# Kernel tuning notes

Hardware: AMD Instinct MI355X
Metric: run time of the kernel (lower is better)

## Reference

```python
import jax, jax.numpy as jnp
import numpy as np

D_MODEL = 1024
HEAD = 16
HEAD_DIM = D_MODEL // HEAD
BATCH = 2
SEQ = 2048


def setup_inputs() -> dict:
    key = jax.random.key(0)
    ks = jax.random.split(key, 11)
    s = 0.02
    return {
        "q": jax.random.normal(ks[0], (BATCH, SEQ, D_MODEL), dtype=jnp.float32),
        "k": jax.random.normal(ks[1], (BATCH, SEQ, D_MODEL), dtype=jnp.float32),
        "v": jax.random.normal(ks[2], (BATCH, SEQ, D_MODEL), dtype=jnp.float32),
        "w_q": jax.random.normal(ks[3], (D_MODEL, D_MODEL), dtype=jnp.float32) * s,
        "b_q": jnp.zeros((D_MODEL,), dtype=jnp.float32),
        "w_k": jax.random.normal(ks[4], (D_MODEL, D_MODEL), dtype=jnp.float32) * s,
        "b_k": jnp.zeros((D_MODEL,), dtype=jnp.float32),
        "w_v": jax.random.normal(ks[5], (D_MODEL, D_MODEL), dtype=jnp.float32) * s,
        "b_v": jnp.zeros((D_MODEL,), dtype=jnp.float32),
        "w_o": jax.random.normal(ks[6], (D_MODEL, D_MODEL), dtype=jnp.float32) * s,
        "b_o": jnp.zeros((D_MODEL,), dtype=jnp.float32),
    }


def reference(q, k, v, w_q, b_q, w_k, b_k, w_v, b_v, w_o, b_o):
    B, S, _ = q.shape
    # linear projections (torch Linear: x @ W^T + b)
    qp = q @ w_q.T + b_q
    kp = k @ w_k.T + b_k
    vp = v @ w_v.T + b_v
    # [B, S, H, Dh] -> [B, H, S, Dh]
    qh = qp.reshape(B, S, HEAD, HEAD_DIM).transpose(0, 2, 1, 3)
    kh = kp.reshape(B, S, HEAD, HEAD_DIM).transpose(0, 2, 1, 3)
    vh = vp.reshape(B, S, HEAD, HEAD_DIM).transpose(0, 2, 1, 3)
    # scaled dot-product attention with explicit score matrix
    scale = 1.0 / jnp.sqrt(jnp.float32(HEAD_DIM))
    scores = jnp.einsum("bhqd,bhkd->bhqk", qh, kh) * scale  # [B,H,S,S]
    attn = jax.nn.softmax(scores, axis=-1)
    z = jnp.einsum("bhqk,bhkd->bhqd", attn, vh)
    z = z.transpose(0, 2, 1, 3).reshape(B, S, D_MODEL)
    z = z @ w_o.T + b_o
    return (z, attn)
```

## Files before the change

kernel.cpp:

```cpp
#include <hip/hip_runtime.h>
#include <hip/hip_bf16.h>
#include <stdint.h>

#define D_MODEL 1024
#define NHEAD   16
#define HDIM    64
#define BATCH   2
#define SEQ     2048
#define BS_TOK  (BATCH*SEQ)

using bf16 = __hip_bfloat16;
typedef __attribute__((ext_vector_type(8))) short frag8;
typedef __attribute__((ext_vector_type(4))) float facc4;
typedef __attribute__((ext_vector_type(4))) float fvec4;

__device__ __forceinline__ void gld_lds16(const void* g, void* l) {
    __builtin_amdgcn_global_load_lds(
        reinterpret_cast<const __attribute__((address_space(1))) uint32_t*>(
            reinterpret_cast<uintptr_t>(g)),
        reinterpret_cast<__attribute__((address_space(3))) uint32_t*>(
            reinterpret_cast<uintptr_t>(l)),
        16, 0, 0);
}

__global__ __launch_bounds__(256) void cvt_multi(const float4* __restrict__ s0, const float4* __restrict__ s1,
                                                 const float4* __restrict__ s2, const float4* __restrict__ s3,
                                                 ushort4* __restrict__ d0, ushort4* __restrict__ d1,
                                                 ushort4* __restrict__ d2, ushort4* __restrict__ d3,
                                                 int n4, int nblk) {
    int t = blockIdx.x / nblk;
    int i = (blockIdx.x - t * nblk) * 256 + threadIdx.x;
    if (i >= n4) return;
    const float4* s = (t == 0) ? s0 : (t == 1) ? s1 : (t == 2) ? s2 : s3;
    ushort4*       d = (t == 0) ? d0 : (t == 1) ? d1 : (t == 2) ? d2 : d3;
    float4 v = s[i];
    bf16 a = __float2bfloat16(v.x), b = __float2bfloat16(v.y),
         c = __float2bfloat16(v.z), e = __float2bfloat16(v.w);
    ushort4 u;
    __builtin_memcpy(&u.x, &a, 2);
    __builtin_memcpy(&u.y, &b, 2);
    __builtin_memcpy(&u.z, &c, 2);
    __builtin_memcpy(&u.w, &e, 2);
    d[i] = u;
}

template<bool OUT_BF16, bool ROW_BIAS>
__device__ __forceinline__ void gemm_core(bf16* AsBuf, bf16* BsBuf,
                                          const bf16* __restrict__ A,
                                          const bf16* __restrict__ Bt,
                                          const float* __restrict__ bias,
                                          void* __restrict__ Cout,
                                          int M, int N, int K, int bx, int by) {
    const int tid  = threadIdx.x;
    const int lane = tid & 63, wave = tid >> 6;
    const int wm = wave >> 1, wn = wave & 1;
    const int L15 = lane & 15, quad = lane >> 4;
    const int m0 = by * 128, n0 = bx * 64;
    const int ar  = tid >> 3;
    const int acS = ((tid & 7) ^ (ar & 7)) * 8;

    const bf16* Agl[4];
    const bf16* Bgl[2];
#pragma unroll
    for (int q = 0; q < 4; q++) Agl[q] = A + (size_t)(m0 + q * 32 + ar) * K + acS;
#pragma unroll
    for (int q = 0; q < 2; q++) Bgl[q] = Bt + (size_t)(n0 + q * 32 + ar) * K + acS;

    const facc4 zero4 = {0.f, 0.f, 0.f, 0.f};
    facc4 acc[4][2];
#pragma unroll
    for (int mt = 0; mt < 4; mt++) { acc[mt][0] = zero4; acc[mt][1] = zero4; }

#define G_STAGE(BUF, KO) do {                                                   \
        _Pragma("unroll")                                                       \
        for (int q = 0; q < 4; q++)                                             \
            gld_lds16(Agl[q] + (KO), AsBuf + (BUF) * 8192 + q * 2048 + wave * 512); \
        _Pragma("unroll")                                                       \
        for (int q = 0; q < 2; q++)                                             \
            gld_lds16(Bgl[q] + (KO), BsBuf + (BUF) * 4096 + q * 2048 + wave * 512); \
    } while (0)

#define G_COMPUTE(BUF) do {                                                     \
        const bf16* Ab = AsBuf + (BUF) * 8192;                                  \
        const bf16* Bb = BsBuf + (BUF) * 4096;                                  \
        _Pragma("unroll")                                                       \
        for (int h = 0; h < 2; h++) {                                           \
            frag8 af[4], bfr[2];                                                \
            _Pragma("unroll")                                                   \
            for (int mt = 0; mt < 4; mt++) {                                    \
                int row = wm * 64 + mt * 16 + L15;                              \
                int c8 = (h * 4 + quad) ^ (row & 7);                            \
                af[mt] = *(const frag8*)(Ab + row * 64 + c8 * 8);               \
            }                                                                   \
            _Pragma("unroll")                                                   \
            for (int nt = 0; nt < 2; nt++) {                                    \
                int row = wn * 32 + nt * 16 + L15;                              \
                int c8 = (h * 4 + quad) ^ (row & 7);                            \
                bfr[nt] = *(const frag8*)(Bb + row * 64 + c8 * 8);              \
            }                                                                   \
            _Pragma("unroll")                                                   \
            for (int mt = 0; mt < 4; mt++)                                      \
                _Pragma("unroll")                                               \
                for (int nt = 0; nt < 2; nt++)                                  \
                    acc[mt][nt] = __builtin_amdgcn_mfma_f32_16x16x32_bf16(af[mt], bfr[nt], acc[mt][nt], 0, 0, 0); \
        }                                                                       \
    } while (0)

    G_STAGE(0, 0);
    __syncthreads();
    int cur = 0;
    for (int k0 = 64; k0 < K; k0 += 64) {
        G_STAGE(cur ^ 1, k0);
        G_COMPUTE(cur);
        __syncthreads();
        cur ^= 1;
    }
    G_COMPUTE(cur);

#pragma unroll
    for (int mt = 0; mt < 4; mt++)
#pragma unroll
        for (int nt = 0; nt < 2; nt++)
#pragma unroll
            for (int r = 0; r < 4; r++) {
                int row = m0 + wm * 64 + mt * 16 + quad * 4 + r;
                int col = n0 + wn * 32 + nt * 16 + L15;
                float v = acc[mt][nt][r] + (ROW_BIAS ? bias[row] : bias[col]);
                if (OUT_BF16) ((bf16*)Cout)[(size_t)row * N + col] = __float2bfloat16(v);
                else          ((float*)Cout)[(size_t)row * N + col] = v;
            }
#undef G_STAGE
#undef G_COMPUTE
}

template<bool OUT_BF16, bool ROW_BIAS>
__global__ __launch_bounds__(256) void gemm_bt(const bf16* __restrict__ A,
                                               const bf16* __restrict__ Bt,
                                               const float* __restrict__ bias,
                                               void* __restrict__ Cout,
                                               int M, int N, int K) {
    __shared__ bf16 As[2 * 8192];
    __shared__ bf16 Bs[2 * 4096];
    gemm_core<OUT_BF16, ROW_BIAS>(As, Bs, A, Bt, bias, Cout, M, N, K, blockIdx.x, blockIdx.y);
}

__global__ __launch_bounds__(256) void gemm_qk(const bf16* __restrict__ qA, const bf16* __restrict__ qW,
                                               const float* __restrict__ qb, bf16* __restrict__ qO,
                                               const bf16* __restrict__ kA, const bf16* __restrict__ kW,
                                               const float* __restrict__ kb, bf16* __restrict__ kO) {
    __shared__ bf16 As[2 * 8192];
    __shared__ bf16 Bs[2 * 4096];
    if (blockIdx.z == 0)
        gemm_core<true, false>(As, Bs, qA, qW, qb, qO, BS_TOK, D_MODEL, D_MODEL, blockIdx.x, blockIdx.y);
    else
        gemm_core<true, false>(As, Bs, kA, kW, kb, kO, BS_TOK, D_MODEL, D_MODEL, blockIdx.x, blockIdx.y);
}

__device__ __forceinline__ int pidx2(int row, int col) {
    int chunk = col >> 3;
    return row * 512 + (((chunk ^ (row & 7)) << 3) | (col & 7));
}

__global__ __launch_bounds__(256) void attn_kernel(const bf16* __restrict__ qp,
                                                   const bf16* __restrict__ kp,
                                                   const bf16* __restrict__ vT,
                                                   bf16* __restrict__ zbuf,
                                                   float* __restrict__ attn_out) {
    __shared__ bf16 ptile[16 * 512];
    __shared__ float sred[4][16];
    __shared__ float sinv[16];
    const int bid0 = blockIdx.x;
    const int bid = (bid0 & 7) * 512 + (bid0 >> 3);
    const int strip = bid & 127, bh = bid >> 7;
    const int b = bh >> 4, h = bh & 15;
    const int i0 = strip * 16;
    const int tid = threadIdx.x, lane = tid & 63, wave = tid >> 6;
    const int L15 = lane & 15, quad = lane >> 4;
    const float scale = 0.125f;

    frag8 aq0, aq1;
    {
        size_t base = (size_t)(b * SEQ + i0 + L15) * D_MODEL + h * HDIM + quad * 8;
        aq0 = *(const frag8*)(qp + base);
        aq1 = *(const frag8*)(qp + base + 32);
    }
    const facc4 zero4 = {0.f, 0.f, 0.f, 0.f};

    float sums[4] = {0.f, 0.f, 0.f, 0.f};
    for (int tt = 0; tt < 32; tt += 2) {
        int j0a = wave * 512 + tt * 16;
        size_t kba = (size_t)(b * SEQ + j0a + L15) * D_MODEL + h * HDIM + quad * 8;
        frag8 a0 = *(const frag8*)(kp + kba);
        frag8 a1 = *(const frag8*)(kp + kba + 32);
        frag8 c0 = *(const frag8*)(kp + kba + (size_t)16 * D_MODEL);
        frag8 c1 = *(const frag8*)(kp + kba + (size_t)16 * D_MODEL + 32);
        facc4 acca = zero4, accb = zero4;
        acca = __builtin_amdgcn_mfma_f32_16x16x32_bf16(aq0, a0, acca, 0, 0, 0);
        accb = __builtin_amdgcn_mfma_f32_16x16x32_bf16(aq0, c0, accb, 0, 0, 0);
        acca = __builtin_amdgcn_mfma_f32_16x16x32_bf16(aq1, a1, acca, 0, 0, 0);
        accb = __builtin_amdgcn_mfma_f32_16x16x32_bf16(aq1, c1, accb, 0, 0, 0);
#pragma unroll
        for (int r = 0; r < 4; r++)
            sums[r] += __expf(acca[r] * scale) + __expf(accb[r] * scale);
    }
#pragma unroll
    for (int m = 1; m <= 8; m <<= 1)
#pragma unroll
        for (int r = 0; r < 4; r++) sums[r] += __shfl_xor(sums[r], m, 64);
    if (L15 == 0) {
#pragma unroll
        for (int r = 0; r < 4; r++) sred[wave][quad * 4 + r] = sums[r];
    }
    __syncthreads();
    if (tid < 16) sinv[tid] = 1.0f / (sred[0][tid] + sred[1][tid] + sred[2][tid] + sred[3][tid]);
    __syncthreads();

    float invr[4];
#pragma unroll
    for (int r = 0; r < 4; r++) invr[r] = sinv[quad * 4 + r];

    facc4 zacc = zero4;
    const bf16* vrow = vT + (size_t)(h * HDIM + wave * 16 + L15) * BS_TOK + b * SEQ;
    const size_t obase = ((size_t)bh * SEQ + i0) * SEQ;

    for (int c = 0; c < 4; c++) {
#pragma unroll 2
        for (int tt = 0; tt < 8; tt++) {
            int jrel = wave * 128 + tt * 16;
            int j0 = c * 512 + jrel;
            size_t kb = (size_t)(b * SEQ + j0 + L15) * D_MODEL + h * HDIM + quad * 8;
            frag8 kf0 = *(const frag8*)(kp + kb);
            frag8 kf1 = *(const frag8*)(kp + kb + 32);
            facc4 acc = zero4;
            acc = __builtin_amdgcn_mfma_f32_16x16x32_bf16(aq0, kf0, acc, 0, 0, 0);
            acc = __builtin_amdgcn_mfma_f32_16x16x32_bf16(aq1, kf1, acc, 0, 0, 0);
            int colw = jrel + L15;
#pragma unroll
            for (int r = 0; r < 4; r++) {
                int row = quad * 4 + r;
                float a = __expf(acc[r] * scale) * invr[r];
                ptile[pidx2(row, colw)] = __float2bfloat16(a);
            }
        }
        __syncthreads();
#pragma unroll
        for (int it = 0; it < 4; it++) {
            int row = it * 4 + wave;
#pragma unroll
            for (int seg = 0; seg < 2; seg++) {
                int colb = seg * 256 + lane * 4;
                int chunk = colb >> 3, sub = colb & 7;
                const bf16* src = &ptile[row * 512 + (((chunk ^ (row & 7)) << 3) | sub)];
                fvec4 o = {__bfloat162float(src[0]), __bfloat162float(src[1]),
                           __bfloat162float(src[2]), __bfloat162float(src[3])};
                __builtin_nontemporal_store(o,
                    (fvec4*)(attn_out + obase + (size_t)row * SEQ + c * 512 + colb));
            }
        }
#pragma unroll 4
        for (int k0 = 0; k0 < 512; k0 += 32) {
            frag8 pa = *(const frag8*)&ptile[L15 * 512 + ((((k0 >> 3) + quad) ^ (L15 & 7)) << 3)];
            frag8 vb = *(const frag8*)(vrow + c * 512 + k0 + quad * 8);
            zacc = __builtin_amdgcn_mfma_f32_16x16x32_bf16(pa, vb, zacc, 0, 0, 0);
        }
        __syncthreads();
    }
#pragma unroll
    for (int r = 0; r < 4; r++) {
        size_t row = (size_t)(b * SEQ + i0 + quad * 4 + r);
        zbuf[row * D_MODEL + h * HDIM + wave * 16 + L15] = __float2bfloat16(zacc[r]);
    }
}

extern "C" void kernel_launch(void* const* d_in, const int* in_sizes, int n_in,
                              void* d_out, int out_size, void* d_ws, size_t ws_size,
                              hipStream_t stream) {
    const float* q   = (const float*)d_in[0];
    const float* k   = (const float*)d_in[1];
    const float* v   = (const float*)d_in[2];
    const float* w_q = (const float*)d_in[3];
    const float* b_q = (const float*)d_in[4];
    const float* w_k = (const float*)d_in[5];
    const float* b_k = (const float*)d_in[6];
    const float* w_v = (const float*)d_in[7];
    const float* b_v = (const float*)d_in[8];
    const float* w_o = (const float*)d_in[9];
    const float* b_o = (const float*)d_in[10];

    char* ws = (char*)d_ws;
    const size_t TOK = (size_t)BS_TOK * D_MODEL;
    const size_t WM  = (size_t)D_MODEL * D_MODEL;
    bf16* qbf  = (bf16*)(ws);
    bf16* kbf  = (bf16*)(ws + 8388608);
    bf16* vbf  = (bf16*)(ws + 16777216);
    bf16* wqb  = (bf16*)(ws + 25165824);
    bf16* wkb  = (bf16*)(ws + 27262976);
    bf16* wvb  = (bf16*)(ws + 29360128);
    bf16* wob  = (bf16*)(ws + 31457280);
    bf16* qp   = (bf16*)(ws + 33554432);
    bf16* kp   = (bf16*)(ws + 41943040);
    bf16* vT   = (bf16*)(ws + 50331648);
    bf16* zbf  = (bf16*)(ws + 58720256);

    float* z_out    = (float*)d_out;
    float* attn_out = (float*)d_out + (size_t)BATCH * SEQ * D_MODEL;

    int n4t = (int)(TOK / 4), n4w = (int)(WM / 4);
    int nbt = (n4t + 255) / 256, nbw = (n4w + 255) / 256;
    cvt_multi<<<3 * nbt, 256, 0, stream>>>((const float4*)q, (const float4*)k, (const float4*)v,
                                           (const float4*)v,
                                           (ushort4*)qbf, (ushort4*)kbf, (ushort4*)vbf,
                                           (ushort4*)vbf, n4t, nbt);
    cvt_multi<<<4 * nbw, 256, 0, stream>>>((const float4*)w_q, (const float4*)w_k,
                                           (const float4*)w_v, (const float4*)w_o,
                                           (ushort4*)wqb, (ushort4*)wkb, (ushort4*)wvb,
                                           (ushort4*)wob, n4w, nbw);

    dim3 gqk(D_MODEL / 64, BS_TOK / 128, 2);
    gemm_qk<<<gqk, 256, 0, stream>>>(qbf, wqb, b_q, qp, kbf, wkb, b_k, kp);
    dim3 g2(BS_TOK / 64, D_MODEL / 128);
    gemm_bt<true, true><<<g2, 256, 0, stream>>>(wvb, vbf, b_v, vT, D_MODEL, BS_TOK, D_MODEL);

    attn_kernel<<<BATCH * NHEAD * (SEQ / 16), 256, 0, stream>>>(qp, kp, vT, zbf, attn_out);

    dim3 g1(D_MODEL / 64, BS_TOK / 128);
    gemm_bt<false, false><<<g1, 256, 0, stream>>>(zbf, wob, b_o, z_out, BS_TOK, D_MODEL, D_MODEL);
}
```

Measured before the change: 913.0 us.

## Merge conversion and projection launches, double-buffer attention P tile

```diff
diff --git a/kernel.cpp b/kernel.cpp
--- a/kernel.cpp
+++ b/kernel.cpp
@@ -12,7 +12,6 @@
 using bf16 = __hip_bfloat16;
 typedef __attribute__((ext_vector_type(8))) short frag8;
 typedef __attribute__((ext_vector_type(4))) float facc4;
-typedef __attribute__((ext_vector_type(4))) float fvec4;
 
 __device__ __forceinline__ void gld_lds16(const void* g, void* l) {
     __builtin_amdgcn_global_load_lds(
@@ -23,19 +22,39 @@
         16, 0, 0);
 }
 
-__global__ __launch_bounds__(256) void cvt_multi(const float4* __restrict__ s0, const float4* __restrict__ s1,
-                                                 const float4* __restrict__ s2, const float4* __restrict__ s3,
-                                                 ushort4* __restrict__ d0, ushort4* __restrict__ d1,
-                                                 ushort4* __restrict__ d2, ushort4* __restrict__ d3,
-                                                 int n4, int nblk) {
-    int t = blockIdx.x / nblk;
-    int i = (blockIdx.x - t * nblk) * 256 + threadIdx.x;
+__device__ __forceinline__ void ldsbar() {
+    asm volatile("s_waitcnt lgkmcnt(0)" ::: "memory");
+    __builtin_amdgcn_sched_barrier(0);
+    __builtin_amdgcn_s_barrier();
+}
+
+__global__ __launch_bounds__(256) void cvt_all(const float* __restrict__ q, const float* __restrict__ k,
+                                               const float* __restrict__ v, const float* __restrict__ wq,
+                                               const float* __restrict__ wk, const float* __restrict__ wv,
+                                               const float* __restrict__ wo,
+                                               ushort* __restrict__ dq, ushort* __restrict__ dk,
+                                               ushort* __restrict__ dv, ushort* __restrict__ dwq,
+                                               ushort* __restrict__ dwk, ushort* __restrict__ dwv,
+                                               ushort* __restrict__ dwo,
+                                               int nbt, int n4t, int nbw, int n4w) {
+    int blk = blockIdx.x;
+    const float4* s; ushort4* d; int i, n4;
+    if (blk < 3 * nbt) {
+        int t = blk / nbt;
+        i = (blk - t * nbt) * 256 + threadIdx.x; n4 = n4t;
+        s = (const float4*)(t == 0 ? q : t == 1 ? k : v);
+        d = (ushort4*)(t == 0 ? dq : t == 1 ? dk : dv);
+    } else {
+        blk -= 3 * nbt;
+        int t = blk / nbw;
+        i = (blk - t * nbw) * 256 + threadIdx.x; n4 = n4w;
+        s = (const float4*)(t == 0 ? wq : t == 1 ? wk : t == 2 ? wv : wo);
+        d = (ushort4*)(t == 0 ? dwq : t == 1 ? dwk : t == 2 ? dwv : dwo);
+    }
     if (i >= n4) return;
-    const float4* s = (t == 0) ? s0 : (t == 1) ? s1 : (t == 2) ? s2 : s3;
-    ushort4*       d = (t == 0) ? d0 : (t == 1) ? d1 : (t == 2) ? d2 : d3;
-    float4 v = s[i];
-    bf16 a = __float2bfloat16(v.x), b = __float2bfloat16(v.y),
-         c = __float2bfloat16(v.z), e = __float2bfloat16(v.w);
+    float4 vv = s[i];
+    bf16 a = __float2bfloat16(vv.x), b = __float2bfloat16(vv.y),
+         c = __float2bfloat16(vv.z), e = __float2bfloat16(vv.w);
     ushort4 u;
     __builtin_memcpy(&u.x, &a, 2);
     __builtin_memcpy(&u.y, &b, 2);
@@ -133,6 +152,26 @@
 #undef G_COMPUTE
 }
 
+__global__ __launch_bounds__(256) void proj_all(const bf16* __restrict__ qA, const bf16* __restrict__ Wq,
+                                                const float* __restrict__ bq, bf16* __restrict__ qO,
+                                                const bf16* __restrict__ kA, const bf16* __restrict__ Wk,
+                                                const float* __restrict__ bk, bf16* __restrict__ kO,
+                                                const bf16* __restrict__ Wv, const bf16* __restrict__ vA,
+                                                const float* __restrict__ bv, bf16* __restrict__ vO) {
+    __shared__ bf16 As[2 * 8192];
+    __shared__ bf16 Bs[2 * 4096];
+    int id = blockIdx.x;
+    if (id < 512) {
+        gemm_core<true, false>(As, Bs, qA, Wq, bq, qO, BS_TOK, D_MODEL, D_MODEL, id & 15, id >> 4);
+    } else if (id < 1024) {
+        id -= 512;
+        gemm_core<true, false>(As, Bs, kA, Wk, bk, kO, BS_TOK, D_MODEL, D_MODEL, id & 15, id >> 4);
+    } else {
+        id -= 1024;
+        gemm_core<true, true>(As, Bs, Wv, vA, bv, vO, D_MODEL, BS_TOK, D_MODEL, id & 63, id >> 6);
+    }
+}
+
 template<bool OUT_BF16, bool ROW_BIAS>
 __global__ __launch_bounds__(256) void gemm_bt(const bf16* __restrict__ A,
                                                const bf16* __restrict__ Bt,
@@ -144,18 +183,6 @@
     gemm_core<OUT_BF16, ROW_BIAS>(As, Bs, A, Bt, bias, Cout, M, N, K, blockIdx.x, blockIdx.y);
 }
 
-__global__ __launch_bounds__(256) void gemm_qk(const bf16* __restrict__ qA, const bf16* __restrict__ qW,
-                                               const float* __restrict__ qb, bf16* __restrict__ qO,
-                                               const bf16* __restrict__ kA, const bf16* __restrict__ kW,
-                                               const float* __restrict__ kb, bf16* __restrict__ kO) {
-    __shared__ bf16 As[2 * 8192];
-    __shared__ bf16 Bs[2 * 4096];
-    if (blockIdx.z == 0)
-        gemm_core<true, false>(As, Bs, qA, qW, qb, qO, BS_TOK, D_MODEL, D_MODEL, blockIdx.x, blockIdx.y);
-    else
-        gemm_core<true, false>(As, Bs, kA, kW, kb, kO, BS_TOK, D_MODEL, D_MODEL, blockIdx.x, blockIdx.y);
-}
-
 __device__ __forceinline__ int pidx2(int row, int col) {
     int chunk = col >> 3;
     return row * 512 + (((chunk ^ (row & 7)) << 3) | (col & 7));
@@ -166,7 +193,7 @@
                                                    const bf16* __restrict__ vT,
                                                    bf16* __restrict__ zbuf,
                                                    float* __restrict__ attn_out) {
-    __shared__ bf16 ptile[16 * 512];
+    __shared__ bf16 ptile[2][16 * 512];
     __shared__ float sred[4][16];
     __shared__ float sinv[16];
     const int bid0 = blockIdx.x;
@@ -223,48 +250,50 @@
     const bf16* vrow = vT + (size_t)(h * HDIM + wave * 16 + L15) * BS_TOK + b * SEQ;
     const size_t obase = ((size_t)bh * SEQ + i0) * SEQ;
 
-    for (int c = 0; c < 4; c++) {
-#pragma unroll 2
-        for (int tt = 0; tt < 8; tt++) {
-            int jrel = wave * 128 + tt * 16;
-            int j0 = c * 512 + jrel;
-            size_t kb = (size_t)(b * SEQ + j0 + L15) * D_MODEL + h * HDIM + quad * 8;
-            frag8 kf0 = *(const frag8*)(kp + kb);
-            frag8 kf1 = *(const frag8*)(kp + kb + 32);
-            facc4 acc = zero4;
-            acc = __builtin_amdgcn_mfma_f32_16x16x32_bf16(aq0, kf0, acc, 0, 0, 0);
-            acc = __builtin_amdgcn_mfma_f32_16x16x32_bf16(aq1, kf1, acc, 0, 0, 0);
-            int colw = jrel + L15;
-#pragma unroll
-            for (int r = 0; r < 4; r++) {
-                int row = quad * 4 + r;
-                float a = __expf(acc[r] * scale) * invr[r];
-                ptile[pidx2(row, colw)] = __float2bfloat16(a);
-            }
-        }
-        __syncthreads();
-#pragma unroll
-        for (int it = 0; it < 4; it++) {
-            int row = it * 4 + wave;
-#pragma unroll
-            for (int seg = 0; seg < 2; seg++) {
-                int colb = seg * 256 + lane * 4;
-                int chunk = colb >> 3, sub = colb & 7;
-                const bf16* src = &ptile[row * 512 + (((chunk ^ (row & 7)) << 3) | sub)];
-                fvec4 o = {__bfloat162float(src[0]), __bfloat162float(src[1]),
-                           __bfloat162float(src[2]), __bfloat162float(src[3])};
-                __builtin_nontemporal_store(o,
-                    (fvec4*)(attn_out + obase + (size_t)row * SEQ + c * 512 + colb));
-            }
-        }
-#pragma unroll 4
-        for (int k0 = 0; k0 < 512; k0 += 32) {
-            frag8 pa = *(const frag8*)&ptile[L15 * 512 + ((((k0 >> 3) + quad) ^ (L15 & 7)) << 3)];
-            frag8 vb = *(const frag8*)(vrow + c * 512 + k0 + quad * 8);
-            zacc = __builtin_amdgcn_mfma_f32_16x16x32_bf16(pa, vb, zacc, 0, 0, 0);
-        }
-        __syncthreads();
-    }
+#define ATT_STAGE(CHK, BUF) do {                                                     \
+        _Pragma("unroll")                                                            \
+        for (int tt = 0; tt < 8; tt++) {                                             \
+            int jrel = wave * 128 + tt * 16;                                         \
+            int j0 = (CHK) * 512 + jrel;                                             \
+            size_t kb = (size_t)(b * SEQ + j0 + L15) * D_MODEL + h * HDIM + quad * 8;\
+            frag8 kf0 = *(const frag8*)(kp + kb);                                    \
+            frag8 kf1 = *(const frag8*)(kp + kb + 32);                               \
+            facc4 acc = zero4;                                                       \
+            acc = __builtin_amdgcn_mfma_f32_16x16x32_bf16(aq0, kf0, acc, 0, 0, 0);   \
+            acc = __builtin_amdgcn_mfma_f32_16x16x32_bf16(aq1, kf1, acc, 0, 0, 0);   \
+            int colw = jrel + L15;                                                   \
+            _Pragma("unroll")                                                        \
+            for (int r = 0; r < 4; r++) {                                            \
+                int row = quad * 4 + r;                                              \
+                float a = __expf(acc[r] * scale) * invr[r];                          \
+                attn_out[obase + (size_t)row * SEQ + j0 + L15] = a;                  \
+                ptile[BUF][pidx2(row, colw)] = __float2bfloat16(a);                  \
+            }                                                                        \
+        }                                                                            \
+    } while (0)
+
+#define ATT_PV(CHK, BUF) do {                                                        \
+        _Pragma("unroll")                                                            \
+        for (int k0 = 0; k0 < 512; k0 += 32) {                                       \
+            frag8 pa = *(const frag8*)&ptile[BUF][L15 * 512 +                        \
+                        ((((k0 >> 3) + quad) ^ (L15 & 7)) << 3)];                    \
+            frag8 vb = *(const frag8*)(vrow + (CHK) * 512 + k0 + quad * 8);          \
+            zacc = __builtin_amdgcn_mfma_f32_16x16x32_bf16(pa, vb, zacc, 0, 0, 0);   \
+        }                                                                            \
+    } while (0)
+
+    ATT_STAGE(0, 0);
+    ldsbar();
+    ATT_STAGE(1, 1); ATT_PV(0, 0);
+    ldsbar();
+    ATT_STAGE(2, 0); ATT_PV(1, 1);
+    ldsbar();
+    ATT_STAGE(3, 1); ATT_PV(2, 0);
+    ldsbar();
+    ATT_PV(3, 1);
+#undef ATT_STAGE
+#undef ATT_PV
+
 #pragma unroll
     for (int r = 0; r < 4; r++) {
         size_t row = (size_t)(b * SEQ + i0 + quad * 4 + r);
@@ -307,19 +336,14 @@
 
     int n4t = (int)(TOK / 4), n4w = (int)(WM / 4);
     int nbt = (n4t + 255) / 256, nbw = (n4w + 255) / 256;
-    cvt_multi<<<3 * nbt, 256, 0, stream>>>((const float4*)q, (const float4*)k, (const float4*)v,
-                                           (const float4*)v,
-                                           (ushort4*)qbf, (ushort4*)kbf, (ushort4*)vbf,
-                                           (ushort4*)vbf, n4t, nbt);
-    cvt_multi<<<4 * nbw, 256, 0, stream>>>((const float4*)w_q, (const float4*)w_k,
-                                           (const float4*)w_v, (const float4*)w_o,
-                                           (ushort4*)wqb, (ushort4*)wkb, (ushort4*)wvb,
-                                           (ushort4*)wob, n4w, nbw);
-
-    dim3 gqk(D_MODEL / 64, BS_TOK / 128, 2);
-    gemm_qk<<<gqk, 256, 0, stream>>>(qbf, wqb, b_q, qp, kbf, wkb, b_k, kp);
-    dim3 g2(BS_TOK / 64, D_MODEL / 128);
-    gemm_bt<true, true><<<g2, 256, 0, stream>>>(wvb, vbf, b_v, vT, D_MODEL, BS_TOK, D_MODEL);
+    cvt_all<<<3 * nbt + 4 * nbw, 256, 0, stream>>>(q, k, v, w_q, w_k, w_v, w_o,
+                                                   (ushort*)qbf, (ushort*)kbf, (ushort*)vbf,
+                                                   (ushort*)wqb, (ushort*)wkb, (ushort*)wvb,
+                                                   (ushort*)wob, nbt, n4t, nbw, n4w);
+
+    proj_all<<<1536, 256, 0, stream>>>(qbf, wqb, b_q, qp,
+                                       kbf, wkb, b_k, kp,
+                                       wvb, vbf, b_v, vT);
 
     attn_kernel<<<BATCH * NHEAD * (SEQ / 16), 256, 0, stream>>>(qp, kp, vT, zbf, attn_out);
 
```

New measurement: 960.7 us. 1.05x slower.
